# Performance work log

Hardware: AMD Instinct MI355X
Metric: run time of the kernel (lower is better)

Reference implementation:

```python
import jax, jax.numpy as jnp
import numpy as np

AT = 4000  # number of alpha steps (from generate_alphas default)


def _alphas(lower=0.01, upper=3.0, at=AT):
    # generate_alphas: alphas[0]=lower; alphas[t-1]=(1-(t-1)/AT)*lower+(t-1)/AT*upper
    t = jnp.arange(1, at + 1, dtype=jnp.float32)
    a = (1.0 - (t - 1.0) / at) * lower + ((t - 1.0) / at) * upper
    return a[:, None]  # [AT, 1]


def setup_inputs() -> dict:
    key = jax.random.key(0)
    k0, k1, k2, k3, k4, k5 = jax.random.split(key, 6)
    N, T, b, p = 50, 4000, 512, 32
    x = jax.random.normal(k0, (b, N, p), dtype=jnp.float32)
    x_i = jax.random.randint(k1, (b, p), 0, T)
    y_i = jax.random.randint(k2, (b,), 0, T)
    g = jax.random.uniform(k3, (N * N, N * N), dtype=jnp.float32)
    # xavier_normal for [N*N, 1]
    std = (2.0 / (N * N + 1)) ** 0.5
    weights = jax.random.normal(k4, (N * N, 1), dtype=jnp.float32) * std
    mus = jax.random.uniform(k5, (T, N), dtype=jnp.float32, minval=0.0, maxval=10.0)
    alphas = _alphas()
    return {"x": x, "x_i": x_i, "y_i": y_i, "g": g,
            "weights": weights, "mus": mus, "alphas": alphas}


def reference(x, x_i, y_i, g, weights, mus, alphas):
    b, N, p = x.shape
    F = g @ (weights ** 2)                          # [N*N, 1]
    W = alphas @ (-F.T)                             # [AT, N*N]
    f = jax.nn.softmax(W.reshape(-1, N, N), axis=-1)  # [AT, N, N]
    mu_y = mus[y_i]                                 # [b, N]
    fx = f[x_i]                                     # [b, p, N, N] gather (dominant traffic)
    a = jnp.transpose(x, (0, 2, 1)) - mus[x_i]      # [b, p, N]
    z = jnp.einsum('bpij,bpj->bpi', fx, a)          # [b, p, N]
    Z = z.sum(axis=1) + p * mu_y                    # loop adds mu_y once per feature p
    return (Z, F)
```

## Files before the change

### kernel.cpp

```cpp
#include <hip/hip_runtime.h>
#include <hip/hip_bf16.h>


#define NB   512
#define NN   50
#define NP   32
#define NNN  2500

__global__ void __launch_bounds__(256) k_F(const float* __restrict__ g,
                                           const float* __restrict__ w,
                                           float* __restrict__ F) {
    const int k = blockIdx.x;
    const float4* __restrict__ row4 = (const float4*)(g + (size_t)k * NNN);
    const float4* __restrict__ w4   = (const float4*)w;
    float s = 0.f;
    for (int m = threadIdx.x; m < NNN / 4; m += 256) {
        float4 gv = row4[m];
        float4 wv = w4[m];
        s += gv.x * (wv.x * wv.x) + gv.y * (wv.y * wv.y)
           + gv.z * (wv.z * wv.z) + gv.w * (wv.w * wv.w);
    }
    #pragma unroll
    for (int off = 32; off; off >>= 1) s += __shfl_down(s, off, 64);
    __shared__ float part[4];
    if ((threadIdx.x & 63) == 0) part[threadIdx.x >> 6] = s;
    __syncthreads();
    if (threadIdx.x == 0) F[k] = part[0] + part[1] + part[2] + part[3];
}

__global__ void __launch_bounds__(256) k_Z(const float* __restrict__ x,
                                           const int* __restrict__ x_i,
                                           const int* __restrict__ y_i,
                                           const float* __restrict__ mus,
                                           const float* __restrict__ alphas,
                                           const float* __restrict__ F,
                                           float* __restrict__ Z) {
    const int bb  = blockIdx.x;
    const int tid = threadIdx.x;

    __shared__ float Fs[NN][NN + 1];
    __shared__ float Fmin[NN];
    __shared__ float a[NP][NN + 1];
    __shared__ float alph[NP];
    __shared__ int   ti[NP];
    __shared__ float zsh[NN];

    for (int idx = tid; idx < NNN; idx += 256) {
        Fs[idx / NN][idx % NN] = F[idx];
    }
    if (tid < NP) {
        int t = x_i[bb * NP + tid];
        ti[tid]   = t;
        alph[tid] = alphas[t];
    }
    if (tid < NN) zsh[tid] = 0.f;
    __syncthreads();

    if (tid < NN) {
        float m = Fs[tid][0];
        #pragma unroll
        for (int j = 1; j < NN; ++j) m = fminf(m, Fs[tid][j]);
        Fmin[tid] = m;
    }
    for (int idx = tid; idx < NN * NP; idx += 256) {
        const int j  = idx >> 5;
        const int pp = idx & 31;
        a[pp][j] = x[(size_t)bb * (NN * NP) + idx] - mus[(size_t)ti[pp] * NN + j];
    }
    __syncthreads();

    for (int q = tid; q < NP * NN; q += 256) {
        const int pp = q / NN;
        const int i  = q - pp * NN;
        const float  alpha = alph[pp];
        const float  fmn   = Fmin[i];
        const float* __restrict__ frow = Fs[i];
        const float* __restrict__ arow = a[pp];
        float num = 0.f, den = 0.f;
        #pragma unroll
        for (int j = 0; j < NN; ++j) {
            float e = __expf(alpha * (fmn - frow[j]));
            num += e * arow[j];
            den += e;
        }
        atomicAdd(&zsh[i], num / den);
    }
    __syncthreads();

    if (tid < NN) {
        Z[bb * NN + tid] = zsh[tid] + 32.f * mus[(size_t)y_i[bb] * NN + tid];
    }
}

extern "C" void kernel_launch(void* const* d_in, const int* in_sizes, int n_in,
                              void* d_out, int out_size, void* d_ws, size_t ws_size,
                              hipStream_t stream) {
    const float* x      = (const float*)d_in[0];
    const int*   x_i    = (const int*)  d_in[1];
    const int*   y_i    = (const int*)  d_in[2];
    const float* g      = (const float*)d_in[3];
    const float* w      = (const float*)d_in[4];
    const float* mus    = (const float*)d_in[5];
    const float* alphas = (const float*)d_in[6];

    float* Z = (float*)d_out;
    float* F = Z + NB * NN;

    k_F<<<NNN, 256, 0, stream>>>(g, w, F);
    k_Z<<<NB,  256, 0, stream>>>(x, x_i, y_i, mus, alphas, F, Z);
}
```

Baseline: 105.5 us.

## Restructure Z kernel: per-lane row in registers, 8 waves, no atomics

The Z kernel now launches 512 threads per block. Each lane holds one softmax row of F, precomputed as differences from the row minimum, in registers, and loops over four features per wave with float4 LDS reads of the activation rows. Rows are padded to 52 with +inf and zero so the vector loops need no tail handling. Shared atomics are replaced by per-wave partial sums reduced at the end. This removes redundant LDS reads of F and the atomic contention, at the cost of 14 idle lanes per wave and higher register pressure.

```diff
diff --git a/kernel.cpp b/kernel.cpp
--- a/kernel.cpp
+++ b/kernel.cpp
@@ -6,6 +6,7 @@
 #define NN   50
 #define NP   32
 #define NNN  2500
+#define FSTR 52
 
 __global__ void __launch_bounds__(256) k_F(const float* __restrict__ g,
                                            const float* __restrict__ w,
@@ -28,67 +29,82 @@
     if (threadIdx.x == 0) F[k] = part[0] + part[1] + part[2] + part[3];
 }
 
-__global__ void __launch_bounds__(256) k_Z(const float* __restrict__ x,
+__global__ void __launch_bounds__(512) k_Z(const float* __restrict__ x,
                                            const int* __restrict__ x_i,
                                            const int* __restrict__ y_i,
                                            const float* __restrict__ mus,
                                            const float* __restrict__ alphas,
                                            const float* __restrict__ F,
                                            float* __restrict__ Z) {
-    const int bb  = blockIdx.x;
-    const int tid = threadIdx.x;
+    const int bb   = blockIdx.x;
+    const int tid  = threadIdx.x;
+    const int wave = tid >> 6;
+    const int lane = tid & 63;
 
-    __shared__ float Fs[NN][NN + 1];
-    __shared__ float Fmin[NN];
-    __shared__ float a[NP][NN + 1];
+    __shared__ float Fs[NN * FSTR];
+    __shared__ float a[NP][FSTR];
     __shared__ float alph[NP];
-    __shared__ int   ti[NP];
-    __shared__ float zsh[NN];
+    __shared__ float zp[8][NN];
 
-    for (int idx = tid; idx < NNN; idx += 256) {
-        Fs[idx / NN][idx % NN] = F[idx];
+    for (int idx = tid; idx < NN * FSTR; idx += 512) {
+        const int r = idx / FSTR, c = idx - r * FSTR;
+        Fs[idx] = (c < NN) ? F[r * NN + c] : __builtin_huge_valf();
     }
     if (tid < NP) {
-        int t = x_i[bb * NP + tid];
-        ti[tid]   = t;
+        const int t = x_i[bb * NP + tid];
         alph[tid] = alphas[t];
+        a[tid][NN] = 0.f; a[tid][NN + 1] = 0.f;
     }
-    if (tid < NN) zsh[tid] = 0.f;
+    for (int idx = tid; idx < NN * NP; idx += 512) {
+        const int j  = idx >> 5;
+        const int pp = idx & 31;
+        const int t  = x_i[bb * NP + pp];
+        a[pp][j] = x[(size_t)bb * (NN * NP) + idx] - mus[(size_t)t * NN + j];
+    }
+    __syncthreads();
+
+    const int row = (lane < NN) ? lane : 0;
+    const float4* __restrict__ frow4 = (const float4*)(Fs + row * FSTR);
+    float4 rv[13];
+    #pragma unroll
+    for (int k = 0; k < 13; ++k) rv[k] = frow4[k];
+    float mn = rv[0].x;
+    #pragma unroll
+    for (int k = 0; k < 13; ++k)
+        mn = fminf(mn, fminf(fminf(rv[k].x, rv[k].y), fminf(rv[k].z, rv[k].w)));
+    float d[FSTR];
+    #pragma unroll
+    for (int k = 0; k < 13; ++k) {
+        d[4 * k + 0] = mn - rv[k].x;
+        d[4 * k + 1] = mn - rv[k].y;
+        d[4 * k + 2] = mn - rv[k].z;
+        d[4 * k + 3] = mn - rv[k].w;
+    }
+
+    float zacc = 0.f;
+    #pragma unroll 1
+    for (int s = 0; s < 4; ++s) {
+        const int pp = (wave << 2) + s;
+        const float al = alph[pp];
+        const float4* __restrict__ arow4 = (const float4*)(a[pp]);
+        float num = 0.f, den = 0.f;
+        #pragma unroll
+        for (int k = 0; k < 13; ++k) {
+            const float4 av = arow4[k];
+            float e0 = __expf(al * d[4 * k + 0]); den += e0; num = fmaf(e0, av.x, num);
+            float e1 = __expf(al * d[4 * k + 1]); den += e1; num = fmaf(e1, av.y, num);
+            float e2 = __expf(al * d[4 * k + 2]); den += e2; num = fmaf(e2, av.z, num);
+            float e3 = __expf(al * d[4 * k + 3]); den += e3; num = fmaf(e3, av.w, num);
+        }
+        zacc += num / den;
+    }
+    if (lane < NN) zp[wave][lane] = zacc;
     __syncthreads();
 
     if (tid < NN) {
-        float m = Fs[tid][0];
-        #pragma unroll
-        for (int j = 1; j < NN; ++j) m = fminf(m, Fs[tid][j]);
-        Fmin[tid] = m;
-    }
-    for (int idx = tid; idx < NN * NP; idx += 256) {
-        const int j  = idx >> 5;
-        const int pp = idx & 31;
-        a[pp][j] = x[(size_t)bb * (NN * NP) + idx] - mus[(size_t)ti[pp] * NN + j];
-    }
-    __syncthreads();
-
-    for (int q = tid; q < NP * NN; q += 256) {
-        const int pp = q / NN;
-        const int i  = q - pp * NN;
-        const float  alpha = alph[pp];
-        const float  fmn   = Fmin[i];
-        const float* __restrict__ frow = Fs[i];
-        const float* __restrict__ arow = a[pp];
-        float num = 0.f, den = 0.f;
-        #pragma unroll
-        for (int j = 0; j < NN; ++j) {
-            float e = __expf(alpha * (fmn - frow[j]));
-            num += e * arow[j];
-            den += e;
-        }
-        atomicAdd(&zsh[i], num / den);
-    }
-    __syncthreads();
-
-    if (tid < NN) {
-        Z[bb * NN + tid] = zsh[tid] + 32.f * mus[(size_t)y_i[bb] * NN + tid];
+        float z = zp[0][tid] + zp[1][tid] + zp[2][tid] + zp[3][tid]
+                + zp[4][tid] + zp[5][tid] + zp[6][tid] + zp[7][tid];
+        Z[bb * NN + tid] = z + 32.f * mus[(size_t)y_i[bb] * NN + tid];
     }
 }
 
@@ -107,5 +123,5 @@
     float* F = Z + NB * NN;
 
     k_F<<<NNN, 256, 0, stream>>>(g, w, F);
-    k_Z<<<NB,  256, 0, stream>>>(x, x_i, y_i, mus, alphas, F, Z);
+    k_Z<<<NB,  512, 0, stream>>>(x, x_i, y_i, mus, alphas, F, Z);
 }
```

Result: faster. 99.47 us (-5.7%).
